# Kernel optimization log

Hardware: AMD Instinct MI355X
Metric: run time of the kernel (lower is better)

The kernel has to match this reference:

```python
import jax, jax.numpy as jnp
import numpy as np

B, N, CIN, COUT, K, P = 32, 3072, 32, 8, 3, 4
N2 = N // P


def _lap(key, n):
    a = jax.random.normal(key, (n, n), dtype=jnp.float32)
    # symmetric, spectral radius ~1 (Chebyshev-rescaled Laplacian stand-in)
    return 0.35 * (a + a.T) / jnp.sqrt(jnp.float32(n))


def setup_inputs() -> dict:
    key = jax.random.key(0)
    ks = iter(jax.random.split(key, 40))
    d = {}
    d['x'] = jax.random.normal(next(ks), (B, N, CIN), dtype=jnp.float32)
    d['L0'] = _lap(next(ks), N)
    d['L1'] = _lap(next(ks), N2)

    def cheb_p(k, cin, cout):
        w = jax.random.normal(k, (K, cin, cout), dtype=jnp.float32) * (1.0 / np.sqrt(K * cin))
        return w, jnp.zeros((cout,), jnp.float32)

    def bn_p(c):
        return jnp.ones((c,), jnp.float32), jnp.zeros((c,), jnp.float32)

    d['w11'], d['b11'] = cheb_p(next(ks), CIN, 64); d['g11'], d['be11'] = bn_p(64)
    d['w13'], d['b13'] = cheb_p(next(ks), 64, 128); d['g13'], d['be13'] = bn_p(128)
    d['wr1'] = jax.random.normal(next(ks), (128, CIN), dtype=jnp.float32) * (1.0 / np.sqrt(CIN))
    d['br1'] = jnp.zeros((128,), jnp.float32)
    d['w21'], d['b21'] = cheb_p(next(ks), 128, 192); d['g21'], d['be21'] = bn_p(192)
    d['w23'], d['b23'] = cheb_p(next(ks), 192, 128); d['g23'], d['be23'] = bn_p(128)
    d['wr2'] = jax.random.normal(next(ks), (128, 128), dtype=jnp.float32) * (1.0 / np.sqrt(128))
    d['br2'] = jnp.zeros((128,), jnp.float32)
    d['uw11'], d['ub11'] = cheb_p(next(ks), 256, 128); d['ug11'], d['ube11'] = bn_p(128)
    d['uw12'], d['ub12'] = cheb_p(next(ks), 128, 64); d['ug12'], d['ube12'] = bn_p(64)
    d['uwr1'] = jax.random.normal(next(ks), (64, 256), dtype=jnp.float32) * (1.0 / np.sqrt(256))
    d['ubr1'] = jnp.zeros((64,), jnp.float32)
    d['uw13'], d['ub13'] = cheb_p(next(ks), 64, COUT)
    return d


def cheb_conv(x, L, W, b):
    # x: [B,n,Cin], L: [n,n], W: [K,Cin,Cout] -> [B,n,Cout]
    x0 = x
    x1 = jnp.einsum('ij,bjc->bic', L, x0)
    xs = [x0, x1]
    for _ in range(2, K):
        xs.append(2.0 * jnp.einsum('ij,bjc->bic', L, xs[-1]) - xs[-2])
    xk = jnp.stack(xs, axis=2)  # [B,n,K,Cin]
    return jnp.einsum('bnkc,kco->bno', xk, W) + b


def bn_relu(y, g, be, eps=1e-5):
    mu = jnp.mean(y, axis=(0, 1), keepdims=True)
    var = jnp.mean(jnp.square(y - mu), axis=(0, 1), keepdims=True)
    return jax.nn.relu((y - mu) * jax.lax.rsqrt(var + eps) * g + be)


def lin1x1(x, W, b):
    # torch Conv1d(cin,cout,1) on [B,C,N] == per-node linear
    return jnp.einsum('bnc,oc->bno', x, W) + b


def pool_max(x):
    b, n, c = x.shape
    r = x.reshape(b, n // P, P, c)
    loc = jnp.argmax(r, axis=2)                       # [B,n/P,C]
    vals = jnp.max(r, axis=2)
    idx = loc + (jnp.arange(n // P) * P)[None, :, None]
    return vals, idx


def unpool_max(vals, idx, n):
    b, np_, c = vals.shape
    out = jnp.zeros((b, n, c), vals.dtype)
    bi = jnp.arange(b)[:, None, None]
    ci = jnp.arange(c)[None, None, :]
    return out.at[bi, idx, ci].set(vals)


def reference(x, L0, L1, w11, b11, g11, be11, w13, b13, g13, be13, wr1, br1,
              w21, b21, g21, be21, w23, b23, g23, be23, wr2, br2,
              uw11, ub11, ug11, ube11, uw12, ub12, ug12, ube12, uwr1, ubr1,
              uw13, ub13):
    e1 = bn_relu(cheb_conv(x, L0, w11, b11), g11, be11)
    e1 = bn_relu(cheb_conv(e1, L0, w13, b13), g13, be13)
    e1 = e1 + lin1x1(x, wr1, br1)
    p, idx1 = pool_max(e1)
    e2 = bn_relu(cheb_conv(p, L1, w21, b21), g21, be21)
    e2 = bn_relu(cheb_conv(e2, L1, w23, b23), g23, be23)
    e2 = e2 + lin1x1(p, wr2, br2)
    u = unpool_max(e2, idx1, N)
    cat = jnp.concatenate([u, e1], axis=2)            # [B,N,256]
    d = bn_relu(cheb_conv(cat, L0, uw11, ub11), ug11, ube11)
    d = bn_relu(cheb_conv(d, L0, uw12, ub12), ug12, ube12)
    d = d + lin1x1(cat, uwr1, ubr1)
    return cheb_conv(d, L0, uw13, ub13)               # [B,N,COUT]
```

## Files before the change

kernel.cpp:

```cpp
#include <hip/hip_runtime.h>

typedef _Float16 f16;
typedef f16    half8 __attribute__((ext_vector_type(8)));
typedef float  f32x4 __attribute__((ext_vector_type(4)));
typedef double f64x4 __attribute__((ext_vector_type(4)));

#define LDH 40

template <int MODE>
__global__ __launch_bounds__(256) void gemm_h(
    const f16* __restrict__ A, const f16* __restrict__ Bg, void* __restrict__ Cg,
    int M, int K, int N, int ldc, long long sB, long long sC)
{
    const f16* B = Bg + (size_t)blockIdx.z * sB;

    __shared__ f16 Ah[128][LDH];
    __shared__ f16 Bt[128][LDH];

    const int tid  = threadIdx.x;
    const int lane = tid & 63;
    const int wv   = tid >> 6;
    const int wm   = wv >> 1, wn = wv & 1;
    const int ln   = lane & 15;
    const int q    = lane >> 4;

    const int row0 = blockIdx.y * 128;
    const int col0 = blockIdx.x * 128;

    const int am = tid >> 1;
    const int ak = (tid & 1) << 4;
    const int bk = tid >> 3;
    const int bn = (tid & 7) << 4;

    const f16* Arow = A + (size_t)(row0 + am) * K + ak;
    const int  cb   = col0 + bn;

    f32x4 acc[4][4];
#pragma unroll
    for (int i = 0; i < 4; ++i)
#pragma unroll
        for (int j = 0; j < 4; ++j) acc[i][j] = (f32x4){0.f, 0.f, 0.f, 0.f};

    uint4 a0 = *(const uint4*)(Arow);
    uint4 a1 = *(const uint4*)(Arow + 8);
    uint4 b0 = make_uint4(0, 0, 0, 0), b1 = make_uint4(0, 0, 0, 0);
    {
        const f16* Brow = B + (size_t)bk * N;
        if (cb + 8  <= N) b0 = *(const uint4*)(Brow + cb);
        if (cb + 16 <= N) b1 = *(const uint4*)(Brow + cb + 8);
    }

    for (int k0 = 0; k0 < K; k0 += 32) {
        __syncthreads();
        *(uint4*)&Ah[am][ak]     = a0;
        *(uint4*)&Ah[am][ak + 8] = a1;
        {
            const f16* h0 = (const f16*)&b0;
            const f16* h1 = (const f16*)&b1;
#pragma unroll
            for (int j = 0; j < 8; ++j) {
                int n = bn + j;
                Bt[n][bk ^ (((n >> 4) & 3) << 3)] = h0[j];
            }
#pragma unroll
            for (int j = 0; j < 8; ++j) {
                int n = bn + 8 + j;
                Bt[n][bk ^ (((n >> 4) & 3) << 3)] = h1[j];
            }
        }
        __syncthreads();

        if (k0 + 32 < K) {
            a0 = *(const uint4*)(Arow + k0 + 32);
            a1 = *(const uint4*)(Arow + k0 + 40);
            const f16* Brow = B + (size_t)(k0 + 32 + bk) * N;
            if (cb + 8  <= N) b0 = *(const uint4*)(Brow + cb);
            if (cb + 16 <= N) b1 = *(const uint4*)(Brow + cb + 8);
        }

        half8 af[4], bf[4];
#pragma unroll
        for (int i = 0; i < 4; ++i)
            af[i] = *(const half8*)&Ah[wm * 64 + i * 16 + ln][q * 8];
#pragma unroll
        for (int j = 0; j < 4; ++j) {
            const int nb = wn * 64 + j * 16 + ln;
            const int sw = ((wn * 4 + j) & 3) << 3;
            bf[j] = *(const half8*)&Bt[nb][(q * 8) ^ sw];
        }
#pragma unroll
        for (int i = 0; i < 4; ++i)
#pragma unroll
            for (int j = 0; j < 4; ++j)
                acc[i][j] = __builtin_amdgcn_mfma_f32_16x16x32_f16(af[i], bf[j], acc[i][j], 0, 0, 0);
    }

    const size_t zoff = (size_t)blockIdx.z * sC;
#pragma unroll
    for (int i = 0; i < 4; ++i) {
#pragma unroll
        for (int j = 0; j < 4; ++j) {
            const int c = col0 + wn * 64 + j * 16 + ln;
            if (c < N) {
#pragma unroll
                for (int t = 0; t < 4; ++t) {
                    const int r = row0 + wm * 64 + i * 16 + q * 4 + t;
                    const size_t o = zoff + (size_t)r * ldc + c;
                    const float v = acc[i][j][t];
                    if (MODE == 0)      ((f16*)Cg)[o] = (f16)v;
                    else if (MODE == 1) ((float*)Cg)[o] = v;
                    else                ((float*)Cg)[o] += v;
                }
            }
        }
    }
}

__global__ void probe_f64_k(int* __restrict__ tbl) {
    int l = threadIdx.x & 63;
    f64x4 z = (f64x4){0.0, 0.0, 0.0, 0.0};
    f64x4 dA = __builtin_amdgcn_mfma_f64_16x16x4f64((double)l, 1.0, z, 0, 0, 0);
    f64x4 dB = __builtin_amdgcn_mfma_f64_16x16x4f64(1.0, (double)l, z, 0, 0, 0);
    int* t = tbl + l * 12;
    {
        int v = (int)dA[0];
        if ((v & 3) == 0) { t[0] = l & 15; t[1] = l >> 4; }
        else              { t[0] = l >> 2; t[1] = l & 3;  }
    }
    {
        int v = (int)dB[0];
        if ((v & 3) == 0) { t[2] = l & 15; t[3] = l >> 4; }
        else              { t[2] = l >> 2; t[3] = l & 3;  }
    }
#pragma unroll
    for (int r = 0; r < 4; ++r) {
        int vA = (int)dA[r];
        t[4 + r] = ((vA & 3) == 0) ? (vA - 96) / 4 : (vA - 6) / 16;
        int vB = (int)dB[r];
        t[8 + r] = ((vB & 3) == 0) ? (vB - 96) / 4 : (vB - 6) / 16;
    }
}

#define LDD 66

__device__ inline void loadA4(const float* p, double* d) {
    float4 v = *(const float4*)p;
    d[0] = v.x; d[1] = v.y; d[2] = v.z; d[3] = v.w;
}
__device__ inline void loadA4(const double* p, double* d) {
    double2 v0 = *(const double2*)p, v1 = *(const double2*)(p + 2);
    d[0] = v0.x; d[1] = v0.y; d[2] = v1.x; d[3] = v1.y;
}

template <typename TA>
__global__ __launch_bounds__(256) void gemm_f64(
    const TA* __restrict__ A, const double* __restrict__ Bg, double* __restrict__ Cg,
    const int* __restrict__ tbl,
    int M, int K, int N, long long sB, long long sC, int accum)
{
    const double* B = Bg + (size_t)blockIdx.z * sB;
    double*       C = Cg + (size_t)blockIdx.z * sC;

    __shared__ double As[16][LDD];
    __shared__ double Bs[16][LDD];

    const int tid  = threadIdx.x;
    const int lane = tid & 63;
    const int wv   = tid >> 6;
    const int m0   = wv << 4;

    const int* tl = tbl + lane * 12;
    const int mA = tl[0], kA = tl[1], nB = tl[2], kB = tl[3];
    int iT[4], jT[4];
#pragma unroll
    for (int r = 0; r < 4; ++r) { iT[r] = tl[4 + r]; jT[r] = tl[8 + r]; }

    const int row0 = blockIdx.y * 64;
    const int col0 = blockIdx.x * 64;

    const int ra = tid >> 2;
    const int ka = (tid & 3) << 2;
    const int kb = tid >> 4;
    const int cb = (tid & 15) << 2;

    const TA* Arow = A + (size_t)(row0 + ra) * K + ka;
    const int cbase = col0 + cb;

    f64x4 acc[4];
#pragma unroll
    for (int j = 0; j < 4; ++j) acc[j] = (f64x4){0.0, 0.0, 0.0, 0.0};

    double av[4];
    double2 bv0 = {0.0, 0.0}, bv1 = {0.0, 0.0};
    loadA4(Arow, av);
    if (cbase < N) {
        bv0 = *(const double2*)(B + (size_t)kb * N + cbase);
        bv1 = *(const double2*)(B + (size_t)kb * N + cbase + 2);
    }

    for (int k0 = 0; k0 < K; k0 += 16) {
        __syncthreads();
        As[ka + 0][ra] = av[0]; As[ka + 1][ra] = av[1];
        As[ka + 2][ra] = av[2]; As[ka + 3][ra] = av[3];
        *(double2*)&Bs[kb][cb]     = bv0;
        *(double2*)&Bs[kb][cb + 2] = bv1;
        __syncthreads();

        if (k0 + 16 < K) {
            loadA4(Arow + k0 + 16, av);
            if (cbase < N) {
                bv0 = *(const double2*)(B + (size_t)(k0 + 16 + kb) * N + cbase);
                bv1 = *(const double2*)(B + (size_t)(k0 + 16 + kb) * N + cbase + 2);
            }
        }

#pragma unroll
        for (int kq = 0; kq < 4; ++kq) {
            const double a = As[(kq << 2) + kA][m0 + mA];
#pragma unroll
            for (int j = 0; j < 4; ++j) {
                const double b = Bs[(kq << 2) + kB][(j << 4) + nB];
                acc[j] = __builtin_amdgcn_mfma_f64_16x16x4f64(a, b, acc[j], 0, 0, 0);
            }
        }
    }

#pragma unroll
    for (int j = 0; j < 4; ++j) {
#pragma unroll
        for (int r = 0; r < 4; ++r) {
            const int c = col0 + (j << 4) + jT[r];
            if (c < N) {
                const int rr = row0 + m0 + iT[r];
                double* p = C + (size_t)rr * N + c;
                double v = acc[j][r];
                if (accum) v += *p;
                *p = v;
            }
        }
    }
}

__global__ void zero_k(float* __restrict__ p, int n) {
    int i = blockIdx.x * blockDim.x + threadIdx.x;
    if (i < n) p[i] = 0.f;
}

__global__ void cast16_k(const float* __restrict__ s, f16* __restrict__ d, int n) {
    int i = blockIdx.x * blockDim.x + threadIdx.x;
    if (i < n) d[i] = (f16)s[i];
}

__global__ void regroup_in64_k(const float* __restrict__ x, double* __restrict__ XT, int total) {
    int i = blockIdx.x * blockDim.x + threadIdx.x;
    if (i >= total) return;
    int c = i & 31;
    int t = i >> 5;
    int n = t % 3072;
    int b = t / 3072;
    XT[((((size_t)(b >> 3) * 3072 + n) << 3) + (b & 7)) * 32 + c] = (double)x[i];
}

__global__ void cheb_combine16_k(const float* __restrict__ w, f16* __restrict__ wa,
                                 f16* __restrict__ wb, f16* __restrict__ wc, int n) {
    int i = blockIdx.x * blockDim.x + threadIdx.x;
    if (i >= n) return;
    float w0 = w[i], w1 = w[n + i], w2 = w[2 * n + i];
    wa[i] = (f16)(w0 - w2); wb[i] = (f16)w1; wc[i] = (f16)(2.f * w2);
}
__global__ void cheb_combine64_k(const float* __restrict__ w, double* __restrict__ wa,
                                 double* __restrict__ wb, double* __restrict__ wc, int n) {
    int i = blockIdx.x * blockDim.x + threadIdx.x;
    if (i >= n) return;
    double w0 = w[i], w1 = w[n + i], w2 = w[2 * n + i];
    wa[i] = w0 - w2; wb[i] = w1; wc[i] = 2.0 * w2;
}

__global__ void transpose_w16_k(const float* __restrict__ w, f16* __restrict__ wt, int R, int Ccol) {
    int i = blockIdx.x * blockDim.x + threadIdx.x;
    if (i >= R * Ccol) return;
    int r = i / Ccol, c = i - r * Ccol;
    wt[(size_t)c * R + r] = (f16)w[i];
}
__global__ void transpose_w64_k(const float* __restrict__ w, double* __restrict__ wt, int R, int Ccol) {
    int i = blockIdx.x * blockDim.x + threadIdx.x;
    if (i >= R * Ccol) return;
    int r = i / Ccol, c = i - r * Ccol;
    wt[(size_t)c * R + r] = (double)w[i];
}

__global__ void bn_reduce_k(const float* __restrict__ X, float* __restrict__ stats,
                            int rows, int ld, int off) {
    int c = threadIdx.x;
    float s = 0.f, s2 = 0.f;
    for (int r = blockIdx.x; r < rows; r += gridDim.x) {
        float v = X[(size_t)r * ld + off + c];
        s += v; s2 += v * v;
    }
    atomicAdd(&stats[c], s);
    atomicAdd(&stats[256 + c], s2);
}
__global__ void bn_apply_k(float* X, const float* __restrict__ stats,
                           const float* __restrict__ g, const float* __restrict__ be,
                           const float* rbias, f16* mirror,
                           int total, int C, float invN, int ld, int off) {
    int i = blockIdx.x * blockDim.x + threadIdx.x;
    if (i >= total) return;
    int c = i % C;
    int row = i / C;
    size_t a = (size_t)row * ld + off + c;
    float mu = stats[c] * invN;
    float var = stats[256 + c] * invN - mu * mu;
    float sc = g[c] * rsqrtf(var + 1e-5f);
    float v = (X[a] - mu) * sc + be[c];
    v = fmaxf(v, 0.f);
    if (rbias) v += rbias[c];
    X[a] = v;
    if (mirror) mirror[a] = (f16)v;
}

__global__ void bn_reduce64_k(const double* __restrict__ X, double* __restrict__ stats,
                              int rows, int ld) {
    int c = threadIdx.x;
    double s = 0.0, s2 = 0.0;
    for (int r = blockIdx.x; r < rows; r += gridDim.x) {
        double v = X[(size_t)r * ld + c];
        s += v; s2 += v * v;
    }
    atomicAdd(&stats[c], s);
    atomicAdd(&stats[256 + c], s2);
}
__global__ void bn_apply64_k(double* X, const double* __restrict__ stats,
                             const float* __restrict__ g, const float* __restrict__ be,
                             const float* rbias, int total, int C, double invN) {
    int i = blockIdx.x * blockDim.x + threadIdx.x;
    if (i >= total) return;
    int c = i % C;
    double mu = stats[c] * invN;
    double var = stats[256 + c] * invN - mu * mu;
    double sc = (double)g[c] / sqrt(var + 1e-5);
    double v = (X[i] - mu) * sc + (double)be[c];
    v = v > 0.0 ? v : 0.0;
    if (rbias) v += (double)rbias[c];
    X[i] = v;
}

__global__ void cast_e1_k(const double* __restrict__ E1, f16* __restrict__ cat, int total) {
    int i = blockIdx.x * blockDim.x + threadIdx.x;
    if (i >= total) return;
    int c = i & 127;
    int row = i >> 7;
    cat[(size_t)row * 256 + 128 + c] = (f16)E1[i];
}

__global__ void pool4_64_k(const double* __restrict__ e1, f16* __restrict__ p,
                           int* __restrict__ idx, int total) {
    int i = blockIdx.x * blockDim.x + threadIdx.x;
    if (i >= total) return;
    int c = i & 127;
    int t = i >> 7;
    int b = t & 7;
    t >>= 3;
    int q = t % 768;
    int g = t / 768;
    size_t base = ((((size_t)g * 3072 + 4 * q) << 3) + b) * 128 + c;
    double best = e1[base];
    int bj = 0;
#pragma unroll
    for (int j = 1; j < 4; ++j) {
        double v = e1[base + (size_t)j * 1024];
        if (v > best) { best = v; bj = j; }
    }
    p[i] = (f16)best;
    idx[i] = 4 * q + bj;
}

__global__ void unpool_cat_k(const float* __restrict__ e2, const int* __restrict__ idx,
                             f16* __restrict__ cat, int total) {
    int i = blockIdx.x * blockDim.x + threadIdx.x;
    if (i >= total) return;
    int c = i & 127;
    int t = i >> 7;
    int b = t & 7;
    t >>= 3;
    int q = t % 768;
    int g = t / 768;
    f16 val = (f16)e2[i];
    int id = idx[i];
    size_t base = ((((size_t)g * 3072 + 4 * q) << 3) + b) * 256 + c;
#pragma unroll
    for (int j = 0; j < 4; ++j)
        cat[base + (size_t)j * 2048] = (4 * q + j == id) ? val : (f16)0.f;
}

__global__ void transpose_out_k(const float* __restrict__ O, const float* __restrict__ bias,
                                float* __restrict__ out, int total) {
    int i = blockIdx.x * blockDim.x + threadIdx.x;
    if (i >= total) return;
    int c = i & 7;
    int t = i >> 3;
    int n = t % 3072;
    int b = t / 3072;
    out[i] = O[((((size_t)(b >> 3) * 3072 + n) << 3) + (b & 7)) * 8 + c] + bias[c];
}

extern "C" void kernel_launch(void* const* d_in, const int* in_sizes, int n_in,
                              void* d_out, int out_size, void* d_ws, size_t ws_size,
                              hipStream_t stream)
{
    (void)in_sizes; (void)n_in; (void)out_size; (void)ws_size;

    const float* x    = (const float*)d_in[0];
    const float* L0   = (const float*)d_in[1];
    const float* L1   = (const float*)d_in[2];
    const float* w11  = (const float*)d_in[3];
    const float* g11  = (const float*)d_in[5];
    const float* be11 = (const float*)d_in[6];
    const float* w13  = (const float*)d_in[7];
    const float* g13  = (const float*)d_in[9];
    const float* be13 = (const float*)d_in[10];
    const float* wr1  = (const float*)d_in[11];
    const float* br1  = (const float*)d_in[12];
    const float* w21  = (const float*)d_in[13];
    const float* g21  = (const float*)d_in[15];
    const float* be21 = (const float*)d_in[16];
    const float* w23  = (const float*)d_in[17];
    const float* g23  = (const float*)d_in[19];
    const float* be23 = (const float*)d_in[20];
    const float* wr2  = (const float*)d_in[21];
    const float* br2  = (const float*)d_in[22];
    const float* uw11 = (const float*)d_in[23];
    const float* ug11 = (const float*)d_in[25];
    const float* ube11= (const float*)d_in[26];
    const float* uw12 = (const float*)d_in[27];
    const float* ug12 = (const float*)d_in[29];
    const float* ube12= (const float*)d_in[30];
    const float* uwr1 = (const float*)d_in[31];
    const float* ubr1 = (const float*)d_in[32];
    const float* uw13 = (const float*)d_in[33];
    const float* ub13 = (const float*)d_in[34];
    float* out = (float*)d_out;

    float* ws = (float*)d_ws;
    size_t off = 0;
    auto alloc = [&](size_t n) { float* p = ws + off; off += (n + 63) & ~(size_t)63; return p; };

    float* R1 = alloc(12582912);
    float* R2 = alloc(25165824);
    float* R3 = alloc(6291456);
    float* R4 = alloc(6291456);
    int*  IDX = (int*)alloc(3145728);
    float* L0f = alloc(4718592);
    float* L1f = alloc(294912);
    float* ST  = alloc(1536);
    int*  TBL  = (int*)alloc(768);

    f16* wa21h = (f16*)alloc(12288); f16* wb21h = (f16*)alloc(12288); f16* wc21h = (f16*)alloc(12288);
    f16* wa23h = (f16*)alloc(12288); f16* wb23h = (f16*)alloc(12288); f16* wc23h = (f16*)alloc(12288);
    f16* wau11h = (f16*)alloc(16384); f16* wbu11h = (f16*)alloc(16384); f16* wcu11h = (f16*)alloc(16384);
    f16* wau12h = (f16*)alloc(4096);  f16* wbu12h = (f16*)alloc(4096);  f16* wcu12h = (f16*)alloc(4096);
    f16* wau13h = (f16*)alloc(256);   f16* wbu13h = (f16*)alloc(256);   f16* wcu13h = (f16*)alloc(256);
    f16* wr2Th  = (f16*)alloc(8192);
    f16* uwr1Th = (f16*)alloc(8192);

    double* wa11_64 = (double*)alloc(4096);
    double* wb11_64 = (double*)alloc(4096);
    double* wc11_64 = (double*)alloc(4096);
    double* wa13_64 = (double*)alloc(16384);
    double* wb13_64 = (double*)alloc(16384);
    double* wc13_64 = (double*)alloc(16384);
    double* wr1T_64 = (double*)alloc(8192);

    f16*    CATh = (f16*)R1;
    double* H1   = (double*)R1;
    float*  D1   = R2;
    float*  H2   = R2;
    float*  Y3   = R2 + 4718592;
    float*  O    = R2;
    float*  H64  = R2 + 12582912;
    f16*    T1h  = (f16*)(R2 + 18874368);
    f16*    T2h  = (f16*)(R2 + 22020096);
    double* E1   = (double*)R2;
    double* XT64 = (double*)R3;
    f16*    H2h  = (f16*)R3;
    f16*    D1h  = (f16*)R3;
    double* T1d  = (double*)R4;
    double* T2d  = (double*)IDX;
    f16*    Ph   = (f16*)R4;
    f16*    H64h = (f16*)(R4 + 1572864);
    f16*    L0h  = (f16*)L0f;
    f16*    L1h  = (f16*)L1f;
    double* ST64 = (double*)(ST + 512);
    float*  RFa  = H64;
    float*  RFb  = R2;

    auto gh = [&](int mode, const f16* A, const f16* B, void* C, int M, int K, int N,
                  int ldc, long long sB, long long sC, int z) {
        dim3 grid((N + 127) / 128, M / 128, z);
        if (mode == 0)      gemm_h<0><<<grid, 256, 0, stream>>>(A, B, C, M, K, N, ldc, sB, sC);
        else if (mode == 1) gemm_h<1><<<grid, 256, 0, stream>>>(A, B, C, M, K, N, ldc, sB, sC);
        else                gemm_h<2><<<grid, 256, 0, stream>>>(A, B, C, M, K, N, ldc, sB, sC);
    };
    auto gemm64f = [&](const float* A, const double* B, double* C, int M, int K, int N,
                       long long sB, long long sC, int z, int accum) {
        dim3 grid((N + 63) / 64, M / 64, z);
        gemm_f64<float><<<grid, 256, 0, stream>>>(A, B, C, TBL, M, K, N, sB, sC, accum);
    };
    auto gemm64d = [&](const double* A, const double* B, double* C, int M, int K, int N, int accum) {
        dim3 grid((N + 63) / 64, M / 64);
        gemm_f64<double><<<grid, 256, 0, stream>>>(A, B, C, TBL, M, K, N, 0, 0, accum);
    };
    auto bn = [&](float* X, int rows, int C, int ld, int offc,
                  const float* gp, const float* bep, const float* rbias, f16* mirror) {
        zero_k<<<2, 256, 0, stream>>>(ST, 512);
        bn_reduce_k<<<384, C, 0, stream>>>(X, ST, rows, ld, offc);
        int total = rows * C;
        bn_apply_k<<<(total + 255) / 256, 256, 0, stream>>>(
            X, ST, gp, bep, rbias, mirror, total, C, 1.f / (float)rows, ld, offc);
    };
    auto bn64 = [&](double* X, int rows, int C,
                    const float* gp, const float* bep, const float* rbias) {
        zero_k<<<4, 256, 0, stream>>>(ST + 512, 1024);
        bn_reduce64_k<<<384, C, 0, stream>>>(X, ST64, rows, C);
        int total = rows * C;
        bn_apply64_k<<<(total + 255) / 256, 256, 0, stream>>>(
            X, ST64, gp, bep, rbias, total, C, 1.0 / (double)rows);
    };
    auto comb16 = [&](const float* w, f16* a, f16* b, f16* c, int n) {
        cheb_combine16_k<<<(n + 255) / 256, 256, 0, stream>>>(w, a, b, c, n);
    };

    probe_f64_k<<<1, 64, 0, stream>>>(TBL);

    cheb_combine64_k<<<8, 256, 0, stream>>>(w11, wa11_64, wb11_64, wc11_64, 2048);
    cheb_combine64_k<<<32, 256, 0, stream>>>(w13, wa13_64, wb13_64, wc13_64, 8192);
    transpose_w64_k<<<16, 256, 0, stream>>>(wr1, wr1T_64, 128, 32);
    regroup_in64_k<<<12288, 256, 0, stream>>>(x, XT64, 3145728);

    gemm64f(L0, XT64, T1d, 3072, 3072, 256, 786432, 786432, 4, 0);
    gemm64f(L0, T1d, T2d, 3072, 3072, 256, 786432, 786432, 4, 0);
    gemm64d(XT64, wa11_64, H1, 98304, 32, 64, 0);
    gemm64d(T1d,  wb11_64, H1, 98304, 32, 64, 1);
    gemm64d(T2d,  wc11_64, H1, 98304, 32, 64, 1);
    bn64(H1, 98304, 64, g11, be11, nullptr);

    for (int h = 0; h < 2; ++h) {
        const double* Hh = H1 + (size_t)h * 3145728;
        double*       Eh = E1 + (size_t)h * 6291456;
        gemm64f(L0, Hh, T1d, 3072, 3072, 512, 1572864, 1572864, 2, 0);
        gemm64f(L0, T1d, T2d, 3072, 3072, 512, 1572864, 1572864, 2, 0);
        gemm64d(Hh,  wa13_64, Eh, 49152, 64, 128, 0);
        gemm64d(T1d, wb13_64, Eh, 49152, 64, 128, 1);
        gemm64d(T2d, wc13_64, Eh, 49152, 64, 128, 1);
    }
    bn64(E1, 98304, 128, g13, be13, br1);
    gemm64d(XT64, wr1T_64, E1, 98304, 32, 128, 1);

    comb16(w21,  wa21h,  wb21h,  wc21h,  24576);
    comb16(w23,  wa23h,  wb23h,  wc23h,  24576);
    comb16(uw11, wau11h, wbu11h, wcu11h, 32768);
    comb16(uw12, wau12h, wbu12h, wcu12h, 8192);
    comb16(uw13, wau13h, wbu13h, wcu13h, 512);
    transpose_w16_k<<<64, 256, 0, stream>>>(wr2, wr2Th, 128, 128);
    transpose_w16_k<<<64, 256, 0, stream>>>(uwr1, uwr1Th, 64, 256);
    cast16_k<<<36864, 256, 0, stream>>>(L0, L0h, 9437184);
    cast16_k<<<2304, 256, 0, stream>>>(L1, L1h, 589824);

    pool4_64_k<<<12288, 256, 0, stream>>>(E1, Ph, IDX, 3145728);
    cast_e1_k<<<49152, 256, 0, stream>>>(E1, CATh, 12582912);

    gh(0, L1h, Ph, T1h, 768, 768, 1024, 1024, 786432, 786432, 4);
    gh(0, L1h, T1h, T2h, 768, 768, 1024, 1024, 786432, 786432, 4);
    gh(1, Ph,  wa21h, H2, 24576, 128, 192, 192, 0, 0, 1);
    gh(2, T1h, wb21h, H2, 24576, 128, 192, 192, 0, 0, 1);
    gh(2, T2h, wc21h, H2, 24576, 128, 192, 192, 0, 0, 1);
    bn(H2, 24576, 192, 192, 0, g21, be21, nullptr, H2h);

    gh(0, L1h, H2h, T1h, 768, 768, 1536, 1536, 1179648, 1179648, 4);
    gh(0, L1h, T1h, T2h, 768, 768, 1536, 1536, 1179648, 1179648, 4);
    gh(1, H2h, wa23h, Y3, 24576, 192, 128, 128, 0, 0, 1);
    gh(2, T1h, wb23h, Y3, 24576, 192, 128, 128, 0, 0, 1);
    gh(2, T2h, wc23h, Y3, 24576, 192, 128, 128, 0, 0, 1);
    bn(Y3, 24576, 128, 128, 0, g23, be23, br2, nullptr);
    gh(2, Ph, wr2Th, Y3, 24576, 128, 128, 128, 0, 0, 1);

    unpool_cat_k<<<12288, 256, 0, stream>>>(Y3, IDX, CATh, 3145728);

    for (int h = 0; h < 2; ++h) {
        const f16* catH = CATh + (size_t)h * 12582912;
        float*     Dh   = D1 + (size_t)h * 6291456;
        gh(0, catH, wcu11h, T2h, 49152, 256, 128, 128, 0, 0, 1);
        gh(1, catH, wbu11h, RFa, 49152, 256, 128, 128, 0, 0, 1);
        gh(2, L0h, T2h, RFa, 3072, 3072, 1024, 1024, 3145728, 3145728, 2);
        cast16_k<<<24576, 256, 0, stream>>>(RFa, T1h, 6291456);
        gh(1, catH, wau11h, Dh, 49152, 256, 128, 128, 0, 0, 1);
        gh(2, L0h, T1h, Dh, 3072, 3072, 1024, 1024, 3145728, 3145728, 2);
    }
    bn(D1, 98304, 128, 128, 0, ug11, ube11, nullptr, D1h);

    gh(0, D1h, wcu12h, T2h, 98304, 128, 64, 64, 0, 0, 1);
    gh(1, D1h, wbu12h, RFb, 98304, 128, 64, 64, 0, 0, 1);
    gh(2, L0h, T2h, RFb, 3072, 3072, 512, 512, 1572864, 1572864, 4);
    cast16_k<<<24576, 256, 0, stream>>>(RFb, T1h, 6291456);
    gh(1, D1h, wau12h, H64, 98304, 128, 64, 64, 0, 0, 1);
    gh(2, L0h, T1h, H64, 3072, 3072, 512, 512, 1572864, 1572864, 4);
    bn(H64, 98304, 64, 64, 0, ug12, ube12, ubr1, nullptr);
    gh(2, CATh, uwr1Th, H64, 98304, 256, 64, 64, 0, 0, 1);
    cast16_k<<<24576, 256, 0, stream>>>(H64, H64h, 6291456);

    gh(0, H64h, wcu13h, T2h, 98304, 64, 8, 8, 0, 0, 1);
    gh(1, H64h, wbu13h, RFa, 98304, 64, 8, 8, 0, 0, 1);
    gh(2, L0h, T2h, RFa, 3072, 3072, 64, 64, 196608, 196608, 4);
    cast16_k<<<3072, 256, 0, stream>>>(RFa, T1h, 786432);
    gh(1, H64h, wau13h, O, 98304, 64, 8, 8, 0, 0, 1);
    gh(2, L0h, T1h, O, 3072, 3072, 64, 64, 196608, 196608, 4);

    transpose_out_k<<<3072, 256, 0, stream>>>(O, ub13, out, 786432);
}
```

Before: 4.382 ms.

## Use wider 128-row f64 GEMM tiles with split-K atomic accumulation for Laplacian products

Adds a new f64 MFMA GEMM kernel for the large L0 products. It uses a 128x64 output tile, so each block reuses its B tile across twice as many rows, and it splits K in two across blockIdx.z. The two partial sums are combined with double-precision atomicAdd into an output that a separate kernel zeroes first. The change aims to cut B-tile traffic and add parallelism, at the cost of an extra zeroing pass, atomic write traffic and a nondeterministic summation order.

```diff
diff --git a/kernel.cpp b/kernel.cpp
--- a/kernel.cpp
+++ b/kernel.cpp
@@ -141,8 +141,6 @@
     }
 }
 
-#define LDD 66
-
 __device__ inline void loadA4(const float* p, double* d) {
     float4 v = *(const float4*)p;
     d[0] = v.x; d[1] = v.y; d[2] = v.z; d[3] = v.w;
@@ -151,6 +149,13 @@
     double2 v0 = *(const double2*)p, v1 = *(const double2*)(p + 2);
     d[0] = v0.x; d[1] = v0.y; d[2] = v1.x; d[3] = v1.y;
 }
+__device__ inline void loadA8(const float* p, double* d) {
+    float4 v0 = *(const float4*)p, v1 = *(const float4*)(p + 4);
+    d[0] = v0.x; d[1] = v0.y; d[2] = v0.z; d[3] = v0.w;
+    d[4] = v1.x; d[5] = v1.y; d[6] = v1.z; d[7] = v1.w;
+}
+
+#define LDD 66
 
 template <typename TA>
 __global__ __launch_bounds__(256) void gemm_f64(
@@ -239,6 +244,103 @@
             }
         }
     }
+}
+
+__global__ __launch_bounds__(256) void gemm_f64w(
+    const float* __restrict__ A, const double* __restrict__ Bg, double* __restrict__ Cg,
+    const int* __restrict__ tbl,
+    int M, int K, int N, long long sB, long long sC, int KS)
+{
+    const int g  = blockIdx.z / KS;
+    const int s  = blockIdx.z % KS;
+    const int Ks = K / KS;
+    const int kbeg = s * Ks;
+
+    const double* B = Bg + (size_t)g * sB;
+    double*       C = Cg + (size_t)g * sC;
+
+    __shared__ double As[16][130];
+    __shared__ double Bs[16][66];
+
+    const int tid  = threadIdx.x;
+    const int lane = tid & 63;
+    const int wv   = tid >> 6;
+    const int m0   = wv << 4;
+
+    const int* tl = tbl + lane * 12;
+    const int mA = tl[0], kA = tl[1], nB = tl[2], kB = tl[3];
+    int iT[4], jT[4];
+#pragma unroll
+    for (int r = 0; r < 4; ++r) { iT[r] = tl[4 + r]; jT[r] = tl[8 + r]; }
+
+    const int row0 = blockIdx.y * 128;
+    const int col0 = blockIdx.x * 64;
+
+    const int ra = tid >> 1;
+    const int ka = (tid & 1) << 3;
+    const int kb = tid >> 4;
+    const int cb = (tid & 15) << 2;
+
+    const float* Arow = A + (size_t)(row0 + ra) * K + kbeg + ka;
+    const int cbase = col0 + cb;
+
+    f64x4 acc[2][4];
+#pragma unroll
+    for (int t = 0; t < 2; ++t)
+#pragma unroll
+        for (int j = 0; j < 4; ++j) acc[t][j] = (f64x4){0.0, 0.0, 0.0, 0.0};
+
+    double av[8];
+    double2 bv0 = {0.0, 0.0}, bv1 = {0.0, 0.0};
+    loadA8(Arow, av);
+    if (cbase < N) {
+        const double* Brow = B + (size_t)(kbeg + kb) * N + cbase;
+        bv0 = *(const double2*)(Brow);
+        bv1 = *(const double2*)(Brow + 2);
+    }
+
+    for (int k0 = 0; k0 < Ks; k0 += 16) {
+        __syncthreads();
+#pragma unroll
+        for (int i = 0; i < 8; ++i) As[ka + i][ra] = av[i];
+        *(double2*)&Bs[kb][cb]     = bv0;
+        *(double2*)&Bs[kb][cb + 2] = bv1;
+        __syncthreads();
+
+        if (k0 + 16 < Ks) {
+            loadA8(Arow + k0 + 16, av);
+            if (cbase < N) {
+                const double* Brow = B + (size_t)(kbeg + k0 + 16 + kb) * N + cbase;
+                bv0 = *(const double2*)(Brow);
+                bv1 = *(const double2*)(Brow + 2);
+            }
+        }
+
+#pragma unroll
+        for (int kq = 0; kq < 4; ++kq) {
+            const double a0 = As[(kq << 2) + kA][m0 + mA];
+            const double a1 = As[(kq << 2) + kA][64 + m0 + mA];
+#pragma unroll
+            for (int j = 0; j < 4; ++j) {
+                const double b = Bs[(kq << 2) + kB][(j << 4) + nB];
+                acc[0][j] = __builtin_amdgcn_mfma_f64_16x16x4f64(a0, b, acc[0][j], 0, 0, 0);
+                acc[1][j] = __builtin_amdgcn_mfma_f64_16x16x4f64(a1, b, acc[1][j], 0, 0, 0);
+            }
+        }
+    }
+
+#pragma unroll
+    for (int t = 0; t < 2; ++t)
+#pragma unroll
+        for (int j = 0; j < 4; ++j)
+#pragma unroll
+            for (int r = 0; r < 4; ++r) {
+                const int c = col0 + (j << 4) + jT[r];
+                if (c < N) {
+                    const int rr = row0 + t * 64 + m0 + iT[r];
+                    atomicAdd(&C[(size_t)rr * N + c], acc[t][j][r]);
+                }
+            }
 }
 
 __global__ void zero_k(float* __restrict__ p, int n) {
@@ -501,10 +603,12 @@
         else if (mode == 1) gemm_h<1><<<grid, 256, 0, stream>>>(A, B, C, M, K, N, ldc, sB, sC);
         else                gemm_h<2><<<grid, 256, 0, stream>>>(A, B, C, M, K, N, ldc, sB, sC);
     };
-    auto gemm64f = [&](const float* A, const double* B, double* C, int M, int K, int N,
-                       long long sB, long long sC, int z, int accum) {
-        dim3 grid((N + 63) / 64, M / 64, z);
-        gemm_f64<float><<<grid, 256, 0, stream>>>(A, B, C, TBL, M, K, N, sB, sC, accum);
+    auto gemm64w = [&](const float* A, const double* B, double* C, int M, int K, int N,
+                       long long sB, long long sC, int groups, int KS) {
+        const long long nfl = 2LL * groups * (long long)M * N;
+        zero_k<<<(int)((nfl + 255) / 256), 256, 0, stream>>>((float*)C, (int)nfl);
+        dim3 grid((N + 63) / 64, M / 128, groups * KS);
+        gemm_f64w<<<grid, 256, 0, stream>>>(A, B, C, TBL, M, K, N, sB, sC, KS);
     };
     auto gemm64d = [&](const double* A, const double* B, double* C, int M, int K, int N, int accum) {
         dim3 grid((N + 63) / 64, M / 64);
@@ -537,8 +641,8 @@
     transpose_w64_k<<<16, 256, 0, stream>>>(wr1, wr1T_64, 128, 32);
     regroup_in64_k<<<12288, 256, 0, stream>>>(x, XT64, 3145728);
 
-    gemm64f(L0, XT64, T1d, 3072, 3072, 256, 786432, 786432, 4, 0);
-    gemm64f(L0, T1d, T2d, 3072, 3072, 256, 786432, 786432, 4, 0);
+    gemm64w(L0, XT64, T1d, 3072, 3072, 256, 786432, 786432, 4, 2);
+    gemm64w(L0, T1d, T2d, 3072, 3072, 256, 786432, 786432, 4, 2);
     gemm64d(XT64, wa11_64, H1, 98304, 32, 64, 0);
     gemm64d(T1d,  wb11_64, H1, 98304, 32, 64, 1);
     gemm64d(T2d,  wc11_64, H1, 98304, 32, 64, 1);
@@ -547,8 +651,8 @@
     for (int h = 0; h < 2; ++h) {
         const double* Hh = H1 + (size_t)h * 3145728;
         double*       Eh = E1 + (size_t)h * 6291456;
-        gemm64f(L0, Hh, T1d, 3072, 3072, 512, 1572864, 1572864, 2, 0);
-        gemm64f(L0, T1d, T2d, 3072, 3072, 512, 1572864, 1572864, 2, 0);
+        gemm64w(L0, Hh, T1d, 3072, 3072, 512, 1572864, 1572864, 2, 2);
+        gemm64w(L0, T1d, T2d, 3072, 3072, 512, 1572864, 1572864, 2, 2);
         gemm64d(Hh,  wa13_64, Eh, 49152, 64, 128, 0);
         gemm64d(T1d, wb13_64, Eh, 49152, 64, 128, 1);
         gemm64d(T2d, wc13_64, Eh, 49152, 64, 128, 1);
```

New measurement: 4.645 ms. 1.06x slower.
